# Optimization experiments

Measured on AMD Instinct MI355X. Metric: run time of the kernel, lower is better.

## Reference

```python
import jax, jax.numpy as jnp
import numpy as np
import math

HAD = 1024  # hadamard_size hard-coded in HiggsLinear

def _hadamard_matrix(n):
    H = np.array([[1.0]], dtype=np.float32)
    while H.shape[0] < n:
        H = np.block([[H, H], [H, -H]])
    return H

# normalized Hadamard (scale = 1/sqrt(1024)); symmetric, so x @ _H == H x per block
_H = jnp.asarray(_hadamard_matrix(HAD) / math.sqrt(HAD))

def setup_inputs() -> dict:
    key = jax.random.key(0)
    k1, k2, k3, k4, k5 = jax.random.split(key, 5)
    in_f, out_f, d, n_codes, tokens = 4096, 4096, 2, 256, 8192
    return {
        "x": jax.random.normal(k1, (tokens, in_f), jnp.float32),
        "codes": jax.random.randint(k2, (out_f, in_f // d), 0, n_codes, jnp.int32),
        "grid": jax.random.normal(k3, (n_codes, d), jnp.float32),
        "scales": jax.random.uniform(k4, (out_f, in_f // HAD), jnp.float32, 0.5, 1.5),
        "bias": jax.random.normal(k5, (out_f,), jnp.float32),
    }

def reference(x, codes, grid, scales, bias):
    d = grid.shape[1]
    out_f = codes.shape[0]
    post = ((HAD - 1) // d + 1) * d  # post_hadamard_size
    # --- dequantize weight: codebook gather + per-hadamard-group scale ---
    W = grid[codes]                               # (out, num_higgs_groups, d)
    W = W.reshape(out_f, -1, post)[..., :HAD]     # (out, n_had_groups, 1024)
    W = W * scales[..., None]
    W = W.reshape(out_f, -1)                      # (out, in)
    # --- blockwise Hadamard transform of input (block = 1024) ---
    nh = x.shape[-1] // HAD
    xh = x.reshape(x.shape[:-1] + (nh, HAD)) @ _H
    xh = xh.reshape(x.shape[:-1] + (nh * HAD,))
    # --- fused dequant matmul equivalent: F.linear(xh, W, bias) ---
    return xh @ W.T + bias
```

## Files before the change

### kernel.cpp

```cpp
#include <hip/hip_runtime.h>

#define M_TOK 8192
#define N_OUT 4096
#define K_IN  4096
#define CVT_BLOCKS ((M_TOK * K_IN) / 2048)
#define DEQ_BLOCKS (N_OUT * 4 / 4)

typedef __bf16 bf16x8 __attribute__((ext_vector_type(8)));
typedef float f32x4 __attribute__((ext_vector_type(4)));

__device__ __forceinline__ unsigned short f2b(float f) {
  union { float f; unsigned u; } c; c.f = f;
  unsigned u = c.u;
  return (unsigned short)((u + 0x7FFFu + ((u >> 16) & 1u)) >> 16);
}

__global__ __launch_bounds__(256) void prep_kernel(const float* __restrict__ x,
                                                   unsigned short* __restrict__ xb,
                                                   const int* __restrict__ codes,
                                                   const float* __restrict__ grid,
                                                   const float* __restrict__ scales,
                                                   unsigned short* __restrict__ Wt) {
  if (blockIdx.x < CVT_BLOCKS) {
    long i = ((long)blockIdx.x * 256 + threadIdx.x) * 8;
    float4 a = *(const float4*)(x + i);
    float4 b = *(const float4*)(x + i + 4);
    union { unsigned short us[8]; uint4 v; } o;
    o.us[0] = f2b(a.x); o.us[1] = f2b(a.y); o.us[2] = f2b(a.z); o.us[3] = f2b(a.w);
    o.us[4] = f2b(b.x); o.us[5] = f2b(b.y); o.us[6] = f2b(b.z); o.us[7] = f2b(b.w);
    *(uint4*)(xb + i) = o.v;
  } else {
    int bid = blockIdx.x - CVT_BLOCKS;
    int wave = threadIdx.x >> 6;
    int lane = threadIdx.x & 63;
    int G = bid * 4 + wave;
    int o = G >> 2;
    int g = G & 3;
    const int* crow = codes + (long)o * 2048 + g * 512 + lane * 8;
    int4 c0 = *(const int4*)crow;
    int4 c1 = *(const int4*)(crow + 4);
    float v[16];
    const float2* g2p = (const float2*)grid;
    float2 t;
    t = g2p[c0.x]; v[0] = t.x;  v[1] = t.y;
    t = g2p[c0.y]; v[2] = t.x;  v[3] = t.y;
    t = g2p[c0.z]; v[4] = t.x;  v[5] = t.y;
    t = g2p[c0.w]; v[6] = t.x;  v[7] = t.y;
    t = g2p[c1.x]; v[8] = t.x;  v[9] = t.y;
    t = g2p[c1.y]; v[10] = t.x; v[11] = t.y;
    t = g2p[c1.z]; v[12] = t.x; v[13] = t.y;
    t = g2p[c1.w]; v[14] = t.x; v[15] = t.y;
#pragma unroll
    for (int s = 1; s < 16; s <<= 1) {
#pragma unroll
      for (int base = 0; base < 16; base++) {
        if (!(base & s)) {
          float a = v[base], b = v[base | s];
          v[base] = a + b;
          v[base | s] = a - b;
        }
      }
    }
#pragma unroll
    for (int m = 1; m <= 32; m <<= 1) {
      bool hi = (lane & m) != 0;
#pragma unroll
      for (int c = 0; c < 16; c++) {
        float p = __shfl_xor(v[c], m, 64);
        v[c] = hi ? p - v[c] : p + v[c];
      }
    }
    float sc = scales[o * 4 + g] * 0.03125f;
    union { unsigned short us[16]; uint4 q[2]; } out;
#pragma unroll
    for (int c = 0; c < 16; c++) out.us[c] = f2b(v[c] * sc);
    unsigned short* wp = Wt + (long)o * 4096 + g * 1024 + lane * 16;
    *(uint4*)wp = out.q[0];
    *(uint4*)(wp + 8) = out.q[1];
  }
}

__device__ __forceinline__ void load16_to_lds(const unsigned short* g, unsigned short* l) {
  __builtin_amdgcn_global_load_lds((const __attribute__((address_space(1))) void*)g,
                                   (__attribute__((address_space(3))) void*)l,
                                   16, 0, 0);
}

__global__ __launch_bounds__(256, 2) void gemm_kernel(const unsigned short* __restrict__ A,
                                                      const unsigned short* __restrict__ B,
                                                      const float* __restrict__ bias,
                                                      float* __restrict__ C) {
  __shared__ unsigned short sA[128 * 64];
  __shared__ unsigned short sB[128 * 64];
  const int bm = blockIdx.y * 128;
  const int bn = blockIdx.x * 128;
  const int tid = threadIdx.x;
  const int wave = tid >> 6;
  const int lane = tid & 63;

  const int srow = lane & 15;
  const int scol = ((lane >> 4) ^ (lane & 3)) * 8;
  const long K = K_IN;
  const unsigned short* Ag0 = A + (long)(bm + wave * 16 + srow) * K + scol;
  const unsigned short* Ag1 = A + (long)(bm + (wave + 4) * 16 + srow) * K + scol;
  const unsigned short* Bg0 = B + (long)(bn + wave * 16 + srow) * K + scol;
  const unsigned short* Bg1 = B + (long)(bn + (wave + 4) * 16 + srow) * K + scol;
  unsigned short* lA0 = &sA[wave * 1024];
  unsigned short* lA1 = &sA[(wave + 4) * 1024];
  unsigned short* lB0 = &sB[wave * 1024];
  unsigned short* lB1 = &sB[(wave + 4) * 1024];

  f32x4 acc[4][4] = {};

  const int achunk = (wave >> 1) * 4;
  const int bchunk = (wave & 1) * 4;
  const int fslot8 = ((((lane >> 4) ^ (lane & 3)) * 16) + (lane & 15)) * 8;

  for (int k0 = 0; k0 < K_IN; k0 += 64) {
    __syncthreads();
    load16_to_lds(Ag0 + k0,      lA0);
    load16_to_lds(Ag0 + k0 + 32, lA0 + 512);
    load16_to_lds(Ag1 + k0,      lA1);
    load16_to_lds(Ag1 + k0 + 32, lA1 + 512);
    load16_to_lds(Bg0 + k0,      lB0);
    load16_to_lds(Bg0 + k0 + 32, lB0 + 512);
    load16_to_lds(Bg1 + k0,      lB1);
    load16_to_lds(Bg1 + k0 + 32, lB1 + 512);
    __syncthreads();
#pragma unroll
    for (int kstep = 0; kstep < 2; kstep++) {
      bf16x8 af[4], bfr[4];
#pragma unroll
      for (int i = 0; i < 4; i++)
        af[i] = *(const bf16x8*)&sA[(achunk + i) * 1024 + kstep * 512 + fslot8];
#pragma unroll
      for (int i = 0; i < 4; i++)
        bfr[i] = *(const bf16x8*)&sB[(bchunk + i) * 1024 + kstep * 512 + fslot8];
#pragma unroll
      for (int mi = 0; mi < 4; mi++)
#pragma unroll
        for (int ni = 0; ni < 4; ni++)
          acc[mi][ni] = __builtin_amdgcn_mfma_f32_16x16x32_bf16(af[mi], bfr[ni], acc[mi][ni], 0, 0, 0);
    }
  }

  const int wm = (wave >> 1) * 64;
  const int wn = (wave & 1) * 64;
  const int cn = lane & 15;
  const int cm = (lane >> 4) * 4;
#pragma unroll
  for (int ni = 0; ni < 4; ni++) {
    const int col = bn + wn + ni * 16 + cn;
    const float bb = bias[col];
#pragma unroll
    for (int mi = 0; mi < 4; mi++) {
#pragma unroll
      for (int r = 0; r < 4; r++) {
        const int row = bm + wm + mi * 16 + cm + r;
        C[(long)row * N_OUT + col] = acc[mi][ni][r] + bb;
      }
    }
  }
}

extern "C" void kernel_launch(void* const* d_in, const int* in_sizes, int n_in,
                              void* d_out, int out_size, void* d_ws, size_t ws_size,
                              hipStream_t stream) {
  const float* x      = (const float*)d_in[0];
  const int*   codes  = (const int*)d_in[1];
  const float* grid   = (const float*)d_in[2];
  const float* scales = (const float*)d_in[3];
  const float* bias   = (const float*)d_in[4];
  float* out = (float*)d_out;

  unsigned short* xb = (unsigned short*)d_ws;
  unsigned short* Wt = xb + (size_t)M_TOK * K_IN;

  prep_kernel<<<CVT_BLOCKS + DEQ_BLOCKS, 256, 0, stream>>>(x, xb, codes, grid, scales, Wt);
  gemm_kernel<<<dim3(N_OUT / 128, M_TOK / 128), 256, 0, stream>>>(xb, Wt, bias, out);
}
```

Baseline: 535.7 us.

## Rewrite GEMM with 256x256 tiles, double-buffered LDS and phased MFMA scheduling

Replaces the 128x128 single-buffered GEMM with a 512-thread, 256x256-tile kernel. The next K-tile is prefetched into a second LDS buffer with global_load_lds while the current one is consumed, and the wait uses a partial vmcnt. Each wave computes 128x64 in four phases separated by barriers, with s_setprio raised around the MFMA blocks and a grouped block swizzle for L2 reuse. This aims to hide global load latency and raise arithmetic intensity, at the cost of 128KB of LDS per block, more barriers, and more accumulator registers that may limit occupancy.

```diff
diff --git a/kernel.cpp b/kernel.cpp
--- a/kernel.cpp
+++ b/kernel.cpp
@@ -3,6 +3,7 @@
 #define M_TOK 8192
 #define N_OUT 4096
 #define K_IN  4096
+#define NT    (K_IN / 64)
 #define CVT_BLOCKS ((M_TOK * K_IN) / 2048)
 #define DEQ_BLOCKS (N_OUT * 4 / 4)
 
@@ -86,77 +87,147 @@
                                    16, 0, 0);
 }
 
-__global__ __launch_bounds__(256, 2) void gemm_kernel(const unsigned short* __restrict__ A,
+__device__ __forceinline__ void phase_barrier() {
+  __builtin_amdgcn_s_barrier();
+  __builtin_amdgcn_sched_barrier(0);
+}
+
+__global__ __launch_bounds__(512, 2) void gemm_kernel(const unsigned short* __restrict__ A,
                                                       const unsigned short* __restrict__ B,
                                                       const float* __restrict__ bias,
                                                       float* __restrict__ C) {
-  __shared__ unsigned short sA[128 * 64];
-  __shared__ unsigned short sB[128 * 64];
-  const int bm = blockIdx.y * 128;
-  const int bn = blockIdx.x * 128;
-  const int tid = threadIdx.x;
+  __shared__ unsigned short sA[2][256 * 64];
+  __shared__ unsigned short sB[2][256 * 64];
+
+  const int wg  = blockIdx.x;
+  const int swz = (wg & 7) * (512 / 8) + (wg >> 3);
+  const int bn  = (swz & 15) * 256;
+  const int bm  = (swz >> 4) * 256;
+
+  const int tid  = threadIdx.x;
   const int wave = tid >> 6;
   const int lane = tid & 63;
-
-  const int srow = lane & 15;
-  const int scol = ((lane >> 4) ^ (lane & 3)) * 8;
+  const int wm   = wave >> 2;
+  const int wn   = wave & 3;
+
   const long K = K_IN;
-  const unsigned short* Ag0 = A + (long)(bm + wave * 16 + srow) * K + scol;
-  const unsigned short* Ag1 = A + (long)(bm + (wave + 4) * 16 + srow) * K + scol;
-  const unsigned short* Bg0 = B + (long)(bn + wave * 16 + srow) * K + scol;
-  const unsigned short* Bg1 = B + (long)(bn + (wave + 4) * 16 + srow) * K + scol;
-  unsigned short* lA0 = &sA[wave * 1024];
-  unsigned short* lA1 = &sA[(wave + 4) * 1024];
-  unsigned short* lB0 = &sB[wave * 1024];
-  unsigned short* lB1 = &sB[(wave + 4) * 1024];
-
-  f32x4 acc[4][4] = {};
-
-  const int achunk = (wave >> 1) * 4;
-  const int bchunk = (wave & 1) * 4;
-  const int fslot8 = ((((lane >> 4) ^ (lane & 3)) * 16) + (lane & 15)) * 8;
-
-  for (int k0 = 0; k0 < K_IN; k0 += 64) {
-    __syncthreads();
-    load16_to_lds(Ag0 + k0,      lA0);
-    load16_to_lds(Ag0 + k0 + 32, lA0 + 512);
-    load16_to_lds(Ag1 + k0,      lA1);
-    load16_to_lds(Ag1 + k0 + 32, lA1 + 512);
-    load16_to_lds(Bg0 + k0,      lB0);
-    load16_to_lds(Bg0 + k0 + 32, lB0 + 512);
-    load16_to_lds(Bg1 + k0,      lB1);
-    load16_to_lds(Bg1 + k0 + 32, lB1 + 512);
-    __syncthreads();
-#pragma unroll
-    for (int kstep = 0; kstep < 2; kstep++) {
-      bf16x8 af[4], bfr[4];
-#pragma unroll
-      for (int i = 0; i < 4; i++)
-        af[i] = *(const bf16x8*)&sA[(achunk + i) * 1024 + kstep * 512 + fslot8];
-#pragma unroll
-      for (int i = 0; i < 4; i++)
-        bfr[i] = *(const bf16x8*)&sB[(bchunk + i) * 1024 + kstep * 512 + fslot8];
-#pragma unroll
-      for (int mi = 0; mi < 4; mi++)
-#pragma unroll
-        for (int ni = 0; ni < 4; ni++)
-          acc[mi][ni] = __builtin_amdgcn_mfma_f32_16x16x32_bf16(af[mi], bfr[ni], acc[mi][ni], 0, 0, 0);
-    }
-  }
-
-  const int wm = (wave >> 1) * 64;
-  const int wn = (wave & 1) * 64;
-  const int cn = lane & 15;
-  const int cm = (lane >> 4) * 4;
+  const unsigned short* aSrc[4];
+  const unsigned short* bSrc[4];
+  unsigned short* aDst[4];
+  unsigned short* bDst[4];
+#pragma unroll
+  for (int j = 0; j < 4; j++) {
+    const int g   = tid + j * 512;
+    const int row = g >> 3;
+    const int cg  = (g & 7) ^ (row & 7);
+    aSrc[j] = A + (long)(bm + row) * K + cg * 8;
+    bSrc[j] = B + (long)(bn + row) * K + cg * 8;
+    aDst[j] = &sA[0][g * 8];
+    bDst[j] = &sB[0][g * 8];
+  }
+
+  const int m7  = lane & 7;
+  const int cb  = lane >> 4;
+  const int r0a = wm * 128 + (lane & 15);
+  const int r0b = wn * 64  + (lane & 15);
+  const int aoff0 = (r0a * 8 + ( cb      ^ m7)) * 8;
+  const int aoff1 = (r0a * 8 + ((cb | 4) ^ m7)) * 8;
+  const int boff0 = (r0b * 8 + ( cb      ^ m7)) * 8;
+  const int boff1 = (r0b * 8 + ((cb | 4) ^ m7)) * 8;
+
+  f32x4 acc[8][4] = {};
+
+#pragma unroll
+  for (int j = 0; j < 4; j++) {
+    load16_to_lds(aSrc[j], aDst[j]);
+    load16_to_lds(bSrc[j], bDst[j]);
+  }
+
+  for (int t = 0; t < NT; t++) {
+    const int p = t & 1;
+    const unsigned short* bufA = &sA[p][0];
+    const unsigned short* bufB = &sB[p][0];
+
+    if (t + 1 < NT) {
+      const int koff = (t + 1) * 64;
+      const int q16  = ((t + 1) & 1) * 16384;
+#pragma unroll
+      for (int j = 0; j < 4; j++) {
+        load16_to_lds(aSrc[j] + koff, aDst[j] + q16);
+        load16_to_lds(bSrc[j] + koff, bDst[j] + q16);
+      }
+      asm volatile("s_waitcnt vmcnt(8)" ::: "memory");
+    } else {
+      asm volatile("s_waitcnt vmcnt(0)" ::: "memory");
+    }
+    phase_barrier();
+
+    bf16x8 a0[4], a1[4], b0[4];
+
+#pragma unroll
+    for (int i = 0; i < 4; i++) b0[i] = *(const bf16x8*)(bufB + boff0 + i * 1024);
+#pragma unroll
+    for (int i = 0; i < 4; i++) a0[i] = *(const bf16x8*)(bufA + aoff0 + i * 1024);
+    phase_barrier();
+    __builtin_amdgcn_s_setprio(1);
+#pragma unroll
+    for (int mi = 0; mi < 4; mi++)
+#pragma unroll
+      for (int ni = 0; ni < 4; ni++)
+        acc[mi][ni] = __builtin_amdgcn_mfma_f32_16x16x32_bf16(a0[mi], b0[ni], acc[mi][ni], 0, 0, 0);
+    __builtin_amdgcn_s_setprio(0);
+    phase_barrier();
+
+#pragma unroll
+    for (int i = 0; i < 4; i++) a1[i] = *(const bf16x8*)(bufA + aoff0 + 4096 + i * 1024);
+    phase_barrier();
+    __builtin_amdgcn_s_setprio(1);
+#pragma unroll
+    for (int mi = 0; mi < 4; mi++)
+#pragma unroll
+      for (int ni = 0; ni < 4; ni++)
+        acc[4 + mi][ni] = __builtin_amdgcn_mfma_f32_16x16x32_bf16(a1[mi], b0[ni], acc[4 + mi][ni], 0, 0, 0);
+    __builtin_amdgcn_s_setprio(0);
+    phase_barrier();
+
+#pragma unroll
+    for (int i = 0; i < 4; i++) b0[i] = *(const bf16x8*)(bufB + boff1 + i * 1024);
+#pragma unroll
+    for (int i = 0; i < 4; i++) a0[i] = *(const bf16x8*)(bufA + aoff1 + i * 1024);
+    phase_barrier();
+    __builtin_amdgcn_s_setprio(1);
+#pragma unroll
+    for (int mi = 0; mi < 4; mi++)
+#pragma unroll
+      for (int ni = 0; ni < 4; ni++)
+        acc[mi][ni] = __builtin_amdgcn_mfma_f32_16x16x32_bf16(a0[mi], b0[ni], acc[mi][ni], 0, 0, 0);
+    __builtin_amdgcn_s_setprio(0);
+    phase_barrier();
+
+#pragma unroll
+    for (int i = 0; i < 4; i++) a1[i] = *(const bf16x8*)(bufA + aoff1 + 4096 + i * 1024);
+    phase_barrier();
+    __builtin_amdgcn_s_setprio(1);
+#pragma unroll
+    for (int mi = 0; mi < 4; mi++)
+#pragma unroll
+      for (int ni = 0; ni < 4; ni++)
+        acc[4 + mi][ni] = __builtin_amdgcn_mfma_f32_16x16x32_bf16(a1[mi], b0[ni], acc[4 + mi][ni], 0, 0, 0);
+    __builtin_amdgcn_s_setprio(0);
+    phase_barrier();
+  }
+
+  const int cn  = lane & 15;
+  const int cm4 = (lane >> 4) * 4;
 #pragma unroll
   for (int ni = 0; ni < 4; ni++) {
-    const int col = bn + wn + ni * 16 + cn;
+    const int col = bn + wn * 64 + ni * 16 + cn;
     const float bb = bias[col];
 #pragma unroll
-    for (int mi = 0; mi < 4; mi++) {
+    for (int mi = 0; mi < 8; mi++) {
 #pragma unroll
       for (int r = 0; r < 4; r++) {
-        const int row = bm + wm + mi * 16 + cm + r;
+        const int row = bm + wm * 128 + mi * 16 + cm4 + r;
         C[(long)row * N_OUT + col] = acc[mi][ni][r] + bb;
       }
     }
@@ -177,5 +248,5 @@
   unsigned short* Wt = xb + (size_t)M_TOK * K_IN;
 
   prep_kernel<<<CVT_BLOCKS + DEQ_BLOCKS, 256, 0, stream>>>(x, xb, codes, grid, scales, Wt);
-  gemm_kernel<<<dim3(N_OUT / 128, M_TOK / 128), 256, 0, stream>>>(xb, Wt, bias, out);
-}
+  gemm_kernel<<<512, 512, 0, stream>>>(xb, Wt, bias, out);
+}
```

Measured after the change: 585.0 us. 9.2% more time.
